# Optimization experiments

Hardware: AMD Instinct MI355X
Metric: run time of the kernel (lower is better)

Reference implementation:

```python
import jax, jax.numpy as jnp
from jax import lax
import numpy as np

WINDOW = 51
HALF = WINDOW // 2  # 25
K_SAUVOLA = 0.2     # skimage threshold_sauvola default k
RGB_W = np.array([0.2989, 0.5870, 0.1140], dtype=np.float32)  # tf.image.rgb_to_grayscale weights


def _window_sum(x, axis):
    """Sliding-window sum of length WINDOW along `axis`, 'same' size, reflect padding.
    O(1) per pixel via cumulative sums (integral-image style), matching the
    uniform_filter-based local statistics in skimage's Sauvola."""
    pad = [(0, 0)] * x.ndim
    pad[axis] = (HALF, HALF)
    xp = jnp.pad(x, pad, mode='reflect')
    cs = jnp.cumsum(xp, axis=axis)
    zshape = list(cs.shape)
    zshape[axis] = 1
    cs = jnp.concatenate([jnp.zeros(zshape, cs.dtype), cs], axis=axis)
    n = cs.shape[axis]
    hi = lax.slice_in_dim(cs, WINDOW, n, axis=axis)
    lo = lax.slice_in_dim(cs, 0, n - WINDOW, axis=axis)
    return hi - lo


def _box_mean(x):
    # separable 51x51 box filter over H (axis 1) and W (axis 2)
    s = _window_sum(_window_sum(x, axis=1), axis=2)
    return s / jnp.asarray(WINDOW * WINDOW, x.dtype)


def setup_inputs() -> dict:
    key = jax.random.key(0)
    inputs = jax.random.uniform(key, (8, 1024, 1024, 3), dtype=jnp.float32)
    return {"inputs": inputs}


def reference(inputs) -> jnp.ndarray:
    # RGB -> grayscale (channels == 3 branch), keep channel dim [B,H,W,1]
    gray = jnp.einsum('bhwc,c->bhw', inputs, jnp.asarray(RGB_W))[..., None]
    # local mean / std over 51x51 window
    m = _box_mean(gray)
    m2 = _box_mean(gray * gray)
    var = jnp.maximum(m2 - m * m, 0.0)
    s = jnp.sqrt(var)
    # skimage default dynamic range: r = 0.5 * (max - min) over the whole array
    r = 0.5 * (jnp.max(gray) - jnp.min(gray))
    thresh = m * (1.0 + K_SAUVOLA * (s / r - 1.0))
    # (gray > thresh) * 1
    return (gray > thresh).astype(jnp.float32)
```

## Files before the change

### kernel.cpp

```cpp
#include <hip/hip_runtime.h>

#define IMW 1024
#define IMH 1024
#define NB  8
#define HALF 25
#define STRIP 32
#define NCELL 64

#define W_R ((double)0.2989f)
#define W_G ((double)0.5870f)
#define W_B ((double)0.1140f)
#define INV_AREA (1.0 / 2601.0)

__device__ __forceinline__ int refl(int i, int n) {
    if (i < 0) i = -i;
    if (i >= n) i = 2 * n - 2 - i;
    return i;
}

__device__ __forceinline__ double wsum(const double* __restrict__ C, int p) {
    int a = p + HALF; if (a > IMW - 1) a = IMW - 1;
    int b = p - HALF - 1;
    double s = C[a] - (b >= 0 ? C[b] : 0.0);
    if (p <= HALF - 1)      s += C[HALF - p] - C[0];
    if (p >= IMW - HALF)    s += C[IMW - 2] - C[2*IMW - 2 - HALF - 1 - p];
    return s;
}

__global__ void k0_init(unsigned long long* cells) {
    cells[threadIdx.x] = ~0ULL;
    cells[NCELL + threadIdx.x] = 0ULL;
}

__global__ __launch_bounds__(256) void k1_rowpass(const float* __restrict__ in,
                                                  float2* __restrict__ hp,
                                                  float* __restrict__ gray,
                                                  unsigned long long* __restrict__ cells) {
    __shared__ double cs1[IMW];
    __shared__ double cs2[IMW];
    __shared__ double wt1[4], wt2[4], bmin[4], bmax[4];
    const int row = blockIdx.x;
    const long long base = (long long)row * IMW;
    const int t = threadIdx.x;
    const int lane = t & 63, w = t >> 6;

    const float4* p4 = (const float4*)(in + base * 3);
    float4 f0 = p4[3*t], f1 = p4[3*t+1], f2 = p4[3*t+2];
    double g0 = (double)f0.x*W_R + (double)f0.y*W_G + (double)f0.z*W_B;
    double g1 = (double)f0.w*W_R + (double)f1.x*W_G + (double)f1.y*W_B;
    double g2 = (double)f1.z*W_R + (double)f1.w*W_G + (double)f2.x*W_B;
    double g3 = (double)f2.y*W_R + (double)f2.z*W_G + (double)f2.w*W_B;

    ((float4*)(gray + base))[t] = make_float4((float)g0, (float)g1, (float)g2, (float)g3);

    double l1_0 = g0, l1_1 = l1_0 + g1, l1_2 = l1_1 + g2, l1_3 = l1_2 + g3;
    double q0 = g0*g0, q1 = g1*g1, q2 = g2*g2, q3 = g3*g3;
    double l2_0 = q0, l2_1 = l2_0 + q1, l2_2 = l2_1 + q2, l2_3 = l2_2 + q3;

    double lmin = fmin(fmin(g0, g1), fmin(g2, g3));
    double lmax = fmax(fmax(g0, g1), fmax(g2, g3));
    for (int off = 32; off; off >>= 1) {
        lmin = fmin(lmin, __shfl_down(lmin, off));
        lmax = fmax(lmax, __shfl_down(lmax, off));
    }
    if (lane == 0) { bmin[w] = lmin; bmax[w] = lmax; }

    double v1 = l1_3, v2 = l2_3;
    for (int off = 1; off < 64; off <<= 1) {
        double u1 = __shfl_up(v1, off);
        double u2 = __shfl_up(v2, off);
        if (lane >= off) { v1 += u1; v2 += u2; }
    }
    if (lane == 63) { wt1[w] = v1; wt2[w] = v2; }
    __syncthreads();
    double e1 = v1 - l1_3, e2 = v2 - l2_3;
    for (int j = 0; j < w; j++) { e1 += wt1[j]; e2 += wt2[j]; }

    double2* c1 = (double2*)&cs1[4*t];
    double2* c2 = (double2*)&cs2[4*t];
    c1[0] = make_double2(e1 + l1_0, e1 + l1_1);
    c1[1] = make_double2(e1 + l1_2, e1 + l1_3);
    c2[0] = make_double2(e2 + l2_0, e2 + l2_1);
    c2[1] = make_double2(e2 + l2_2, e2 + l2_3);

    if (t == 0) {
        double m0 = fmin(fmin(bmin[0], bmin[1]), fmin(bmin[2], bmin[3]));
        double m1 = fmax(fmax(bmax[0], bmax[1]), fmax(bmax[2], bmax[3]));
        int cell = row & (NCELL - 1);
        atomicMin(&cells[cell], (unsigned long long)__double_as_longlong(m0));
        atomicMax(&cells[NCELL + cell], (unsigned long long)__double_as_longlong(m1));
    }
    __syncthreads();

    for (int k = 0; k < 4; k++) {
        int p = t + 256 * k;
        hp[base + p] = make_float2((float)wsum(cs1, p), (float)wsum(cs2, p));
    }
}

__global__ __launch_bounds__(256) void k2_colpass(const float* __restrict__ gray,
                                                  const float2* __restrict__ hp,
                                                  const unsigned long long* __restrict__ cells,
                                                  float* __restrict__ out) {
    __shared__ double sr[2];
    const int t = threadIdx.x;
    if (t < 64) {
        unsigned long long mn = cells[t];
        unsigned long long mx = cells[NCELL + t];
        for (int off = 32; off; off >>= 1) {
            unsigned long long a = __shfl_down(mn, off);
            unsigned long long b = __shfl_down(mx, off);
            mn = (a < mn) ? a : mn;
            mx = (b > mx) ? b : mx;
        }
        if (t == 0) {
            sr[0] = __longlong_as_double((long long)mn);
            sr[1] = __longlong_as_double((long long)mx);
        }
    }
    __syncthreads();
    const double r  = 0.5 * (sr[1] - sr[0]);
    const double r2 = r * r;

    const int id   = blockIdx.x;
    const int b    = id & 7;
    const int rest = id >> 3;
    const int ys   = rest & 31;
    const int xc   = rest >> 5;
    const int x  = xc * 256 + t;
    const int y0 = ys * STRIP;
    const long long ib = (long long)b * IMH * IMW;

    double vx = 0.0, vy = 0.0;
    #pragma unroll 8
    for (int j = -HALF; j <= HALF; j++) {
        int ry = refl(y0 + j, IMH);
        float2 h = hp[ib + (long long)ry * IMW + x];
        vx += (double)h.x; vy += (double)h.y;
    }

    #pragma unroll 8
    for (int y = y0; y < y0 + STRIP; y++) {
        long long pix = ib + (long long)y * IMW + x;
        double g = (double)gray[pix];

        double m  = vx * INV_AREA;
        double va = fmax(vy * INV_AREA - m * m, 0.0);
        double A  = g - 0.8 * m;
        int o = (A > 0.0) && (A * A * r2 > 0.04 * m * m * va);
        out[pix] = o ? 1.0f : 0.0f;

        int ra = refl(y + HALF + 1, IMH);
        int rs = refl(y - HALF, IMH);
        float2 ha = hp[ib + (long long)ra * IMW + x];
        float2 hs = hp[ib + (long long)rs * IMW + x];
        vx += (double)ha.x - (double)hs.x;
        vy += (double)ha.y - (double)hs.y;
    }
}

extern "C" void kernel_launch(void* const* d_in, const int* in_sizes, int n_in,
                              void* d_out, int out_size, void* d_ws, size_t ws_size,
                              hipStream_t stream) {
    const float* in = (const float*)d_in[0];
    float* out = (float*)d_out;

    unsigned long long* cells = (unsigned long long*)d_ws;
    float2* hp = (float2*)((char*)d_ws + 4096);
    float* gray = (float*)((char*)d_ws + 4096
                           + (size_t)NB * IMH * IMW * sizeof(float2));

    hipLaunchKernelGGL(k0_init, dim3(1), dim3(NCELL), 0, stream, cells);
    hipLaunchKernelGGL(k1_rowpass, dim3(NB * IMH), dim3(256), 0, stream,
                       in, hp, gray, cells);
    hipLaunchKernelGGL(k2_colpass, dim3((IMW / 256) * (IMH / STRIP) * NB), dim3(256), 0, stream,
                       gray, hp, cells, out);
}
```

Baseline: 206.5 us.

## Halve column strip, use 32-bit min/max atomics, vectorize row-pass stores

Shrinks the column-pass strip from 32 to 16 rows, doubling the block count for better occupancy at the cost of more window-priming reads per strip. Switches the global min/max reduction from 64-bit double atomics to 32-bit float atomics on non-negative float bit patterns. Also writes the horizontal-pass results as float4 pairs instead of float2 to widen global stores.

```diff
diff --git a/kernel.cpp b/kernel.cpp
--- a/kernel.cpp
+++ b/kernel.cpp
@@ -4,7 +4,7 @@
 #define IMH 1024
 #define NB  8
 #define HALF 25
-#define STRIP 32
+#define STRIP 16
 #define NCELL 64
 
 #define W_R ((double)0.2989f)
@@ -27,18 +27,18 @@
     return s;
 }
 
-__global__ void k0_init(unsigned long long* cells) {
-    cells[threadIdx.x] = ~0ULL;
-    cells[NCELL + threadIdx.x] = 0ULL;
+__global__ void k0_init(unsigned* cells) {
+    cells[threadIdx.x] = (threadIdx.x < NCELL) ? 0xFFFFFFFFu : 0u;
 }
 
 __global__ __launch_bounds__(256) void k1_rowpass(const float* __restrict__ in,
                                                   float2* __restrict__ hp,
                                                   float* __restrict__ gray,
-                                                  unsigned long long* __restrict__ cells) {
+                                                  unsigned* __restrict__ cells) {
     __shared__ double cs1[IMW];
     __shared__ double cs2[IMW];
-    __shared__ double wt1[4], wt2[4], bmin[4], bmax[4];
+    __shared__ double wt1[4], wt2[4];
+    __shared__ float bmin[4], bmax[4];
     const int row = blockIdx.x;
     const long long base = (long long)row * IMW;
     const int t = threadIdx.x;
@@ -50,18 +50,18 @@
     double g1 = (double)f0.w*W_R + (double)f1.x*W_G + (double)f1.y*W_B;
     double g2 = (double)f1.z*W_R + (double)f1.w*W_G + (double)f2.x*W_B;
     double g3 = (double)f2.y*W_R + (double)f2.z*W_G + (double)f2.w*W_B;
+    float gf0 = (float)g0, gf1 = (float)g1, gf2 = (float)g2, gf3 = (float)g3;
 
-    ((float4*)(gray + base))[t] = make_float4((float)g0, (float)g1, (float)g2, (float)g3);
+    ((float4*)(gray + base))[t] = make_float4(gf0, gf1, gf2, gf3);
 
     double l1_0 = g0, l1_1 = l1_0 + g1, l1_2 = l1_1 + g2, l1_3 = l1_2 + g3;
-    double q0 = g0*g0, q1 = g1*g1, q2 = g2*g2, q3 = g3*g3;
-    double l2_0 = q0, l2_1 = l2_0 + q1, l2_2 = l2_1 + q2, l2_3 = l2_2 + q3;
+    double l2_0 = g0*g0, l2_1 = l2_0 + g1*g1, l2_2 = l2_1 + g2*g2, l2_3 = l2_2 + g3*g3;
 
-    double lmin = fmin(fmin(g0, g1), fmin(g2, g3));
-    double lmax = fmax(fmax(g0, g1), fmax(g2, g3));
+    float lmin = fminf(fminf(gf0, gf1), fminf(gf2, gf3));
+    float lmax = fmaxf(fmaxf(gf0, gf1), fmaxf(gf2, gf3));
     for (int off = 32; off; off >>= 1) {
-        lmin = fmin(lmin, __shfl_down(lmin, off));
-        lmax = fmax(lmax, __shfl_down(lmax, off));
+        lmin = fminf(lmin, __shfl_down(lmin, off));
+        lmax = fmaxf(lmax, __shfl_down(lmax, off));
     }
     if (lane == 0) { bmin[w] = lmin; bmax[w] = lmax; }
 
@@ -84,38 +84,40 @@
     c2[1] = make_double2(e2 + l2_2, e2 + l2_3);
 
     if (t == 0) {
-        double m0 = fmin(fmin(bmin[0], bmin[1]), fmin(bmin[2], bmin[3]));
-        double m1 = fmax(fmax(bmax[0], bmax[1]), fmax(bmax[2], bmax[3]));
+        float m0 = fminf(fminf(bmin[0], bmin[1]), fminf(bmin[2], bmin[3]));
+        float m1 = fmaxf(fmaxf(bmax[0], bmax[1]), fmaxf(bmax[2], bmax[3]));
         int cell = row & (NCELL - 1);
-        atomicMin(&cells[cell], (unsigned long long)__double_as_longlong(m0));
-        atomicMax(&cells[NCELL + cell], (unsigned long long)__double_as_longlong(m1));
+        atomicMin(&cells[cell], __float_as_uint(m0));
+        atomicMax(&cells[NCELL + cell], __float_as_uint(m1));
     }
     __syncthreads();
 
-    for (int k = 0; k < 4; k++) {
-        int p = t + 256 * k;
-        hp[base + p] = make_float2((float)wsum(cs1, p), (float)wsum(cs2, p));
+    for (int k = 0; k < 2; k++) {
+        int p = 2*t + 512*k;
+        float4 h = make_float4((float)wsum(cs1, p),   (float)wsum(cs2, p),
+                               (float)wsum(cs1, p+1), (float)wsum(cs2, p+1));
+        ((float4*)hp)[(base + p) >> 1] = h;
     }
 }
 
 __global__ __launch_bounds__(256) void k2_colpass(const float* __restrict__ gray,
                                                   const float2* __restrict__ hp,
-                                                  const unsigned long long* __restrict__ cells,
+                                                  const unsigned* __restrict__ cells,
                                                   float* __restrict__ out) {
     __shared__ double sr[2];
     const int t = threadIdx.x;
     if (t < 64) {
-        unsigned long long mn = cells[t];
-        unsigned long long mx = cells[NCELL + t];
+        unsigned mn = cells[t];
+        unsigned mx = cells[NCELL + t];
         for (int off = 32; off; off >>= 1) {
-            unsigned long long a = __shfl_down(mn, off);
-            unsigned long long b = __shfl_down(mx, off);
+            unsigned a = __shfl_down(mn, off);
+            unsigned b = __shfl_down(mx, off);
             mn = (a < mn) ? a : mn;
             mx = (b > mx) ? b : mx;
         }
         if (t == 0) {
-            sr[0] = __longlong_as_double((long long)mn);
-            sr[1] = __longlong_as_double((long long)mx);
+            sr[0] = (double)__uint_as_float(mn);
+            sr[1] = (double)__uint_as_float(mx);
         }
     }
     __syncthreads();
@@ -125,8 +127,8 @@
     const int id   = blockIdx.x;
     const int b    = id & 7;
     const int rest = id >> 3;
-    const int ys   = rest & 31;
-    const int xc   = rest >> 5;
+    const int ys   = rest & 63;
+    const int xc   = rest >> 6;
     const int x  = xc * 256 + t;
     const int y0 = ys * STRIP;
     const long long ib = (long long)b * IMH * IMW;
@@ -165,12 +167,12 @@
     const float* in = (const float*)d_in[0];
     float* out = (float*)d_out;
 
-    unsigned long long* cells = (unsigned long long*)d_ws;
+    unsigned* cells = (unsigned*)d_ws;
     float2* hp = (float2*)((char*)d_ws + 4096);
     float* gray = (float*)((char*)d_ws + 4096
                            + (size_t)NB * IMH * IMW * sizeof(float2));
 
-    hipLaunchKernelGGL(k0_init, dim3(1), dim3(NCELL), 0, stream, cells);
+    hipLaunchKernelGGL(k0_init, dim3(1), dim3(2 * NCELL), 0, stream, cells);
     hipLaunchKernelGGL(k1_rowpass, dim3(NB * IMH), dim3(256), 0, stream,
                        in, hp, gray, cells);
     hipLaunchKernelGGL(k2_colpass, dim3((IMW / 256) * (IMH / STRIP) * NB), dim3(256), 0, stream,
```

Result: slower. 221.1 us (+7.1%).
